# Kernel tuning notes

Hardware: AMD Instinct MI355X
Metric: run time of the kernel (lower is better)

## Reference

```python
import jax, jax.numpy as jnp
import numpy as np

B, M, N, P, H, W, D, DIMG, NH = 32, 2048, 512, 16, 640, 640, 256, 384, 8
PD = 3 * P * P  # 768 flattened patch dim


def layer_norm(x, g, b, eps=1e-5):
    mu = x.mean(-1, keepdims=True)
    var = ((x - mu) ** 2).mean(-1, keepdims=True)
    return (x - mu) * jax.lax.rsqrt(var + eps) * g + b


def get_patches(img, kpts, patch):
    # img [B,3,H,W], kpts [B,N,2] (x,y), NaN rows -> NaN patches
    Bb, C, Hh, Ww = img.shape
    half = patch // 2
    safe = jnp.nan_to_num(kpts, nan=0.0)
    ctr = jnp.round(safe).astype(jnp.int32)
    x0 = jnp.clip(ctr[..., 0] - half, 0, Ww - patch)
    y0 = jnp.clip(ctr[..., 1] - half, 0, Hh - patch)
    offs = jnp.arange(patch)
    ys = y0[..., None] + offs  # [B,N,P]
    xs = x0[..., None] + offs  # [B,N,P]

    def ext(im_b, ys_b, xs_b):
        p = im_b[:, ys_b[:, :, None], xs_b[:, None, :]]  # [C,N,P,P]
        return jnp.transpose(p, (1, 0, 2, 3))  # [N,C,P,P]

    patches = jax.vmap(ext)(img, ys, xs)  # [B,N,C,P,P]
    invalid = jnp.isnan(kpts).any(-1)
    return jnp.where(invalid[:, :, None, None, None], jnp.nan, patches)


def setup_inputs() -> dict:
    key = jax.random.key(0)
    ks = jax.random.split(key, 16)
    im0 = jax.random.uniform(ks[0], (B, 3, H, W), jnp.float32)
    im1 = jax.random.uniform(ks[1], (B, 3, H, W), jnp.float32)
    wh = jnp.array([W - 1.0, H - 1.0], jnp.float32)
    kpts0 = jax.random.uniform(ks[2], (B, M, 2), jnp.float32) * wh
    kpts1 = jax.random.uniform(ks[3], (B, M, 2), jnp.float32) * wh
    scores0 = jax.random.uniform(ks[4], (B, M), jnp.float32)
    scores1 = jax.random.uniform(ks[5], (B, M), jnp.float32)
    image_embs = jax.random.normal(ks[6], (B, DIMG), jnp.float32)
    m0 = jax.random.randint(ks[7], (B, N), 0, M)
    m1 = jax.random.randint(ks[8], (B, N), -300, M)
    m1 = jnp.where(m1 < 0, -1, m1)
    sorted_matches = jnp.stack([m0, m1], axis=-1).astype(jnp.int32)
    s = 0.02
    params = dict(
        ln1_g=jnp.ones((PD,), jnp.float32), ln1_b=jnp.zeros((PD,), jnp.float32),
        W_pe=jax.random.normal(ks[9], (D - 1, PD), jnp.float32) * s,
        b_pe=jnp.zeros((D - 1,), jnp.float32),
        ln2_g=jnp.ones((D - 1,), jnp.float32), ln2_b=jnp.zeros((D - 1,), jnp.float32),
        W_proj=jax.random.normal(ks[10], (D, DIMG), jnp.float32) * s,
        b_proj=jnp.zeros((D,), jnp.float32),
        in_w=jax.random.normal(ks[11], (3 * D, D), jnp.float32) * s,
        in_b=jnp.zeros((3 * D,), jnp.float32),
        out_w=jax.random.normal(ks[12], (D, D), jnp.float32) * s,
        out_b=jnp.zeros((D,), jnp.float32),
        W_fc=jax.random.normal(ks[13], (6, D), jnp.float32) * s,
        b_fc=jnp.zeros((6,), jnp.float32),
    )
    return dict(im0=im0, im1=im1, kpts0=kpts0, kpts1=kpts1, scores0=scores0,
                scores1=scores1, image_embs=image_embs,
                sorted_matches=sorted_matches, **params)


def reference(im0, im1, kpts0, kpts1, scores0, scores1, image_embs,
              sorted_matches, ln1_g, ln1_b, W_pe, b_pe, ln2_g, ln2_b,
              W_proj, b_proj, in_w, in_b, out_w, out_b, W_fc, b_fc):
    im0 = jnp.clip(im0, 0.0, 1.0)
    im1 = jnp.clip(im1, 0.0, 1.0)
    m0 = sorted_matches[..., 0]
    m1 = sorted_matches[..., 1]
    valid = m1 > -1  # [B,N]
    m0c = jnp.clip(m0, 0, M - 1)
    m1c = jnp.clip(m1, 0, M - 1)
    # vectorized masked gather with NaN padding (replaces the double python loop)
    g0 = jnp.take_along_axis(kpts0, m0c[..., None], axis=1)  # [B,N,2]
    g1 = jnp.take_along_axis(kpts1, m1c[..., None], axis=1)
    k0v = jnp.where(valid[..., None], g0, jnp.nan)
    k1v = jnp.where(valid[..., None], g1, jnp.nan)
    s0v = jnp.where(valid, jnp.take_along_axis(scores0, m0c, axis=1), 0.0)
    s1v = jnp.where(valid, jnp.take_along_axis(scores1, m1c, axis=1), 0.0)
    p0 = jnp.nan_to_num(get_patches(im0, k0v, P), nan=-1.0)  # [B,N,3,P,P]
    p1 = jnp.nan_to_num(get_patches(im1, k1v, P), nan=-1.0)
    patches = jnp.concatenate([p0, p1], axis=1)  # [B,2N,3,P,P]
    flat = patches.reshape(B, 2 * N, PD)
    e = layer_norm(flat, ln1_g, ln1_b)
    e = e @ W_pe.T + b_pe
    e = layer_norm(e, ln2_g, ln2_b)  # [B,2N,D-1]
    scores = jnp.concatenate([s0v, s1v], axis=1)  # [B,2N]
    pe = jnp.concatenate([e, scores[..., None]], axis=-1)  # [B,2N,D]
    # motion estimator: cross-attn, query = projected image embedding
    q = image_embs @ W_proj.T + b_proj  # [B,D]
    Wq, Wk, Wv = in_w[:D], in_w[D:2 * D], in_w[2 * D:]
    bq, bk, bv = in_b[:D], in_b[D:2 * D], in_b[2 * D:]
    dh = D // NH
    qh = (q @ Wq.T + bq).reshape(B, 1, NH, dh)
    kh = (pe @ Wk.T + bk).reshape(B, 2 * N, NH, dh)
    vh = (pe @ Wv.T + bv).reshape(B, 2 * N, NH, dh)
    scale = 1.0 / np.sqrt(dh).astype(np.float32)
    att = jnp.einsum('bqhd,bkhd->bhqk', qh, kh) * scale
    a = jax.nn.softmax(att, axis=-1)
    o = jnp.einsum('bhqk,bkhd->bqhd', a, vh).reshape(B, 1, D)
    o = o @ out_w.T + out_b
    out = (o @ W_fc.T + b_fc).reshape(B, 6)
    return out
```

## Files before the change

### kernel.cpp

```cpp
#include <hip/hip_runtime.h>
#include <math.h>

#define BB 32
#define MM 2048
#define NN 512
#define PSZ 16
#define HH 640
#define WW 640
#define DD 256
#define DIMG_ 384
#define NHEADS 8
#define PD_ 768
#define TWO_N 1024
#define ROWS_TOT (BB * TWO_N)
#define CHCT 32

typedef short bf16x8 __attribute__((ext_vector_type(8)));
typedef float f32x4  __attribute__((ext_vector_type(4)));

__device__ __forceinline__ unsigned short f2bf(float x) {
  unsigned int u = __float_as_uint(x);
  u = (u + 0x7FFF + ((u >> 16) & 1)) >> 16;
  return (unsigned short)u;
}
__device__ __forceinline__ float bf2f(unsigned short h) {
  return __uint_as_float(((unsigned int)h) << 16);
}

__device__ __forceinline__ void gload_lds16(const void* g, void* l) {
  __builtin_amdgcn_global_load_lds(
      (const __attribute__((address_space(1))) void*)g,
      (__attribute__((address_space(3))) void*)l, 16, 0, 0);
}

__global__ __launch_bounds__(256) void prep_extract_kernel(
    const float* __restrict__ W_pe,
    unsigned short* __restrict__ Whi, unsigned short* __restrict__ Wlo,
    const float* __restrict__ image_embs,
    const float* __restrict__ W_proj, const float* __restrict__ b_proj,
    const float* __restrict__ in_w,   const float* __restrict__ in_b,
    const float* __restrict__ b_pe,
    const float* __restrict__ ln2_g, const float* __restrict__ ln2_b,
    unsigned short* __restrict__ Vhi, unsigned short* __restrict__ Vlo,
    float* __restrict__ Pc,
    const float* __restrict__ im0, const float* __restrict__ im1,
    const float* __restrict__ kpts0, const float* __restrict__ kpts1,
    const float* __restrict__ scores0, const float* __restrict__ scores1,
    const int*   __restrict__ sorted_matches,
    const float* __restrict__ ln1_g, const float* __restrict__ ln1_b,
    unsigned short* __restrict__ Ahi, unsigned short* __restrict__ Alo,
    float* __restrict__ score_all)
{
  __shared__ float q1[DD];
  __shared__ float q2s[DD];
  __shared__ float u_sh[NHEADS][DD];
  __shared__ float gu_sh[DD][NHEADS];
  __shared__ float sred[NHEADS][3][4];
  const int t = threadIdx.x;

  if (blockIdx.x < 768) {
    const int idx = blockIdx.x * 256 + t;
    const int row = idx / PD_;
    float v = (row < 255) ? W_pe[idx] : 0.0f;
    const unsigned short h = f2bf(v);
    Whi[idx] = h;
    Wlo[idx] = f2bf(v - bf2f(h));
    return;
  }

  if (blockIdx.x < 800) {
    const int b = blockIdx.x - 768;
    {
      const float4* emb = (const float4*)(image_embs + (size_t)b * DIMG_);
      const float4* wr  = (const float4*)(W_proj + (size_t)t * DIMG_);
      float a = b_proj[t];
      #pragma unroll 4
      for (int i = 0; i < DIMG_ / 4; ++i) {
        const float4 e4 = emb[i], w4 = wr[i];
        a += e4.x * w4.x + e4.y * w4.y + e4.z * w4.z + e4.w * w4.w;
      }
      q1[t] = a;
    }
    __syncthreads();
    {
      const float4* wr = (const float4*)(in_w + (size_t)t * DD);
      const float4* qq = (const float4*)q1;
      float a = in_b[t];
      #pragma unroll 4
      for (int i = 0; i < DD / 4; ++i) {
        const float4 q4 = qq[i], w4 = wr[i];
        a += q4.x * w4.x + q4.y * w4.y + q4.z * w4.z + q4.w * w4.w;
      }
      q2s[t] = a;
    }
    __syncthreads();
    #pragma unroll
    for (int h = 0; h < NHEADS; ++h) {
      float s = 0.0f;
      #pragma unroll 8
      for (int i = 0; i < 32; ++i)
        s += q2s[h * 32 + i] * in_w[(size_t)(DD + h * 32 + i) * DD + t];
      u_sh[h][t] = s;
    }
    float ubv = 0.0f;
    if (t < NHEADS) {
      for (int i = 0; i < 32; ++i) ubv += q2s[t * 32 + i] * in_b[DD + t * 32 + i];
    }
    __syncthreads();

    const bool cvld = (t < 255);
    const float g_c = cvld ? ln2_g[t] : 0.0f;
    const float bb_c = cvld ? ln2_b[t] : 0.0f;
    const float pp_c = cvld ? b_pe[t]  : 0.0f;
    const int wv = t >> 6, ln = t & 63;
    #pragma unroll
    for (int h = 0; h < NHEADS; ++h) {
      const float u_c = u_sh[h][t];
      const float gu  = g_c * u_c;
      gu_sh[t][h] = gu;
      float x1 = gu, x2 = bb_c * u_c, x3 = pp_c * gu;
      #pragma unroll
      for (int m = 32; m; m >>= 1) {
        x1 += __shfl_xor(x1, m); x2 += __shfl_xor(x2, m); x3 += __shfl_xor(x3, m);
      }
      if (ln == 0) { sred[h][0][wv] = x1; sred[h][1][wv] = x2; sred[h][2][wv] = x3; }
    }
    __syncthreads();
    if (t < NHEADS) {
      const float S1 = sred[t][0][0] + sred[t][0][1] + sred[t][0][2] + sred[t][0][3];
      const float S2 = sred[t][1][0] + sred[t][1][1] + sred[t][1][2] + sred[t][1][3];
      const float S3 = sred[t][2][0] + sred[t][2][1] + sred[t][2][2] + sred[t][2][3];
      float* pc = Pc + b * 40;
      pc[t]      = S1;
      pc[8 + t]  = S2;
      pc[16 + t] = S3;
      pc[24 + t] = u_sh[t][255];
      pc[32 + t] = ubv;
    }

    #pragma unroll
    for (int kk = 0; kk < 3; ++kk) {
      const int k = t + 256 * kk;
      float vh[NHEADS] = {0, 0, 0, 0, 0, 0, 0, 0};
      for (int c = 0; c < 255; ++c) {
        const float wv_ = W_pe[(size_t)c * PD_ + k];
        const float4 g0 = *(const float4*)&gu_sh[c][0];
        const float4 g1 = *(const float4*)&gu_sh[c][4];
        vh[0] += wv_ * g0.x; vh[1] += wv_ * g0.y; vh[2] += wv_ * g0.z; vh[3] += wv_ * g0.w;
        vh[4] += wv_ * g1.x; vh[5] += wv_ * g1.y; vh[6] += wv_ * g1.z; vh[7] += wv_ * g1.w;
      }
      #pragma unroll
      for (int h = 0; h < NHEADS; ++h) {
        const unsigned short hi = f2bf(vh[h]);
        Vhi[((size_t)b * 16 + h) * PD_ + k] = hi;
        Vlo[((size_t)b * 16 + h) * PD_ + k] = f2bf(vh[h] - bf2f(hi));
      }
      #pragma unroll
      for (int h = NHEADS; h < 16; ++h) {
        Vhi[((size_t)b * 16 + h) * PD_ + k] = 0;
        Vlo[((size_t)b * 16 + h) * PD_ + k] = 0;
      }
    }
    return;
  }

  const int L  = t & 63;
  const long gp = (long)(blockIdx.x - 800) * 4 + (t >> 6);
  const int b   = (int)(gp >> 10);
  const int n2  = (int)(gp & 1023);
  const bool side1 = (n2 >= NN);
  const float* img  = side1 ? im1 : im0;
  const float* kpts = side1 ? kpts1 : kpts0;
  const float* scrs = side1 ? scores1 : scores0;

  const int n  = side1 ? (n2 - NN) : n2;
  const int m0 = sorted_matches[((size_t)b * NN + n) * 2 + 0];
  const int m1 = sorted_matches[((size_t)b * NN + n) * 2 + 1];
  const bool valid = (m1 > -1);
  int midx = side1 ? m1 : m0;
  midx = min(max(midx, 0), MM - 1);
  const float kx = kpts[((size_t)b * MM + midx) * 2 + 0];
  const float ky = kpts[((size_t)b * MM + midx) * 2 + 1];
  const int x0 = min(max((int)rintf(kx) - 8, 0), WW - PSZ);
  const int y0 = min(max((int)rintf(ky) - 8, 0), HH - PSZ);

  float v[12];
  if (valid) {
    const size_t imb = (size_t)b * 3 * HH * WW;
    const int px = (2 * L) & 15;
    #pragma unroll
    for (int j = 0; j < 6; ++j) {
      const int p0 = 2 * L + 128 * j;
      const int c  = p0 >> 8;
      const int py = (p0 >> 4) & 15;
      const float* rp = img + imb + ((size_t)c * HH + y0 + py) * WW + x0 + px;
      v[2 * j]     = fminf(fmaxf(rp[0], 0.0f), 1.0f);
      v[2 * j + 1] = fminf(fmaxf(rp[1], 0.0f), 1.0f);
    }
  } else {
    #pragma unroll
    for (int i = 0; i < 12; ++i) v[i] = -1.0f;
  }

  float s = 0.0f, ss = 0.0f;
  #pragma unroll
  for (int i = 0; i < 12; ++i) { s += v[i]; ss += v[i] * v[i]; }
  #pragma unroll
  for (int m = 32; m; m >>= 1) { s += __shfl_xor(s, m); ss += __shfl_xor(ss, m); }
  const float mu  = s * (1.0f / 768.0f);
  const float var = ss * (1.0f / 768.0f) - mu * mu;
  const float rs  = 1.0f / sqrtf(var + 1e-5f);

  unsigned int* AhiW = (unsigned int*)(Ahi + gp * PD_);
  unsigned int* AloW = (unsigned int*)(Alo + gp * PD_);
  #pragma unroll
  for (int j = 0; j < 6; ++j) {
    const int p0 = 2 * L + 128 * j;
    const float y0e = (v[2 * j]     - mu) * rs * ln1_g[p0]     + ln1_b[p0];
    const float y1e = (v[2 * j + 1] - mu) * rs * ln1_g[p0 + 1] + ln1_b[p0 + 1];
    const unsigned short h0 = f2bf(y0e), h1 = f2bf(y1e);
    AhiW[p0 >> 1] = (unsigned int)h0 | ((unsigned int)h1 << 16);
    const unsigned short l0 = f2bf(y0e - bf2f(h0));
    const unsigned short l1 = f2bf(y1e - bf2f(h1));
    AloW[p0 >> 1] = (unsigned int)l0 | ((unsigned int)l1 << 16);
  }
  if (L == 0) {
    score_all[gp] = valid ? scrs[(size_t)b * MM + midx] : 0.0f;
  }
}

__global__ __launch_bounds__(256, 2) void gemm_fused_kernel(
    const unsigned short* __restrict__ Ahi, const unsigned short* __restrict__ Alo,
    const unsigned short* __restrict__ Whi, const unsigned short* __restrict__ Wlo,
    const unsigned short* __restrict__ Vhi, const unsigned short* __restrict__ Vlo,
    const float* __restrict__ b_pe,
    const float* __restrict__ ln2_g, const float* __restrict__ ln2_b,
    const float* __restrict__ score_all,
    const float* __restrict__ Pc,
    float* __restrict__ pe, float* __restrict__ lt)
{
  __shared__ __align__(16) unsigned short sm[21504];
  const int t = threadIdx.x;
  const int w = t >> 6, L = t & 63;
  const int mt = blockIdx.x;
  const int bidx = mt >> 4;

  const int rr   = L >> 2;
  const int q_st = (L & 3) ^ ((L >> 4) & 3);
  const int lane_m = L & 15, quad = L >> 4;
  const int swz = quad ^ (lane_m >> 2);

  const unsigned short* gsrc[11];
  int ldst[11];
  #pragma unroll
  for (int c = 0; c < 11; ++c) {
    const int cc = w + 4 * c;
    const unsigned short* sp = Ahi; long rb = 0; int dst = 0;
    if (cc < 4)       { sp = Ahi; rb = (long)mt * 64 + cc * 16;       dst = cc * 512; }
    else if (cc < 8)  { sp = Alo; rb = (long)mt * 64 + (cc - 4) * 16; dst = 2048 + (cc - 4) * 512; }
    else if (cc < 25) { const int r0 = (cc - 8) * 16;
                        sp = (r0 < 256) ? (Whi + (long)r0 * PD_)
                                        : (Vhi + (long)bidx * 16 * PD_);
                        dst = 4096 + (cc - 8) * 512; }
    else if (cc < 42) { const int r0 = (cc - 25) * 16;
                        sp = (r0 < 256) ? (Wlo + (long)r0 * PD_)
                                        : (Vlo + (long)bidx * 16 * PD_);
                        dst = 12800 + (cc - 25) * 512; }
    gsrc[c] = sp + (rb + rr) * (long)PD_ + q_st * 8;
    ldst[c] = dst;
  }
  const int CNT = (w < 2) ? 11 : 10;
  const int JW  = (w == 3) ? 5 : 4;

  f32x4 acc[4][5];
  #pragma unroll
  for (int i = 0; i < 4; ++i)
    #pragma unroll
    for (int j = 0; j < 5; ++j) acc[i][j] = (f32x4){0.f, 0.f, 0.f, 0.f};

  for (int ks = 0; ks < PD_ / 32; ++ks) {
    const int k0 = ks * 32;
    __syncthreads();
    #pragma unroll
    for (int c = 0; c < 11; ++c)
      if (c < CNT) gload_lds16(gsrc[c] + k0, sm + ldst[c]);
    __syncthreads();

    bf16x8 ah[4], al[4];
    #pragma unroll
    for (int i = 0; i < 4; ++i) {
      const int offa = (i * 16 + lane_m) * 32 + swz * 8;
      ah[i] = *(const bf16x8*)(sm + offa);
      al[i] = *(const bf16x8*)(sm + 2048 + offa);
    }
    #pragma unroll
    for (int j = 0; j < 5; ++j) {
      if (j < JW) {
        const int offb = (w * 64 + j * 16 + lane_m) * 32 + swz * 8;
        const bf16x8 bh = *(const bf16x8*)(sm + 4096 + offb);
        const bf16x8 bl = *(const bf16x8*)(sm + 12800 + offb);
        #pragma unroll
        for (int i = 0; i < 4; ++i) {
          acc[i][j] = __builtin_amdgcn_mfma_f32_16x16x32_bf16(ah[i], bh, acc[i][j], 0, 0, 0);
          acc[i][j] = __builtin_amdgcn_mfma_f32_16x16x32_bf16(ah[i], bl, acc[i][j], 0, 0, 0);
          acc[i][j] = __builtin_amdgcn_mfma_f32_16x16x32_bf16(al[i], bh, acc[i][j], 0, 0, 0);
        }
      }
    }
  }

  __syncthreads();
  float* const fs = (float*)sm;
  float p4[4], g4[4], b4[4];
  #pragma unroll
  for (int j = 0; j < 4; ++j) {
    const int c = w * 64 + j * 16 + lane_m;
    const bool cv = (c < 255);
    p4[j] = cv ? b_pe[c]  : 0.0f;
    g4[j] = cv ? ln2_g[c] : 0.0f;
    b4[j] = cv ? ln2_b[c] : 0.0f;
  }
  float sv[16], qv[16];
  #pragma unroll
  for (int i = 0; i < 4; ++i)
    #pragma unroll
    for (int v = 0; v < 4; ++v) {
      float s = 0.0f, q = 0.0f;
      #pragma unroll
      for (int j = 0; j < 4; ++j) {
        const float x = acc[i][j][v] + p4[j];
        s += x; q += x * x;
      }
      sv[i * 4 + v] = s; qv[i * 4 + v] = q;
    }
  #pragma unroll
  for (int iv = 0; iv < 16; ++iv) {
    #pragma unroll
    for (int m = 1; m <= 8; m <<= 1) {
      sv[iv] += __shfl_xor(sv[iv], m);
      qv[iv] += __shfl_xor(qv[iv], m);
    }
  }
  if (lane_m == 0) {
    #pragma unroll
    for (int i = 0; i < 4; ++i)
      #pragma unroll
      for (int v = 0; v < 4; ++v) {
        const int row = i * 16 + quad * 4 + v;
        fs[w * 64 + row]       = sv[i * 4 + v];
        fs[256 + w * 64 + row] = qv[i * 4 + v];
      }
  }
  __syncthreads();
  if (t < 64) {
    const float S  = fs[t] + fs[64 + t] + fs[128 + t] + fs[192 + t];
    const float SS = fs[256 + t] + fs[320 + t] + fs[384 + t] + fs[448 + t];
    const float mu  = S * (1.0f / 255.0f);
    const float var = SS * (1.0f / 255.0f) - mu * mu;
    fs[512 + t] = mu;
    fs[576 + t] = 1.0f / sqrtf(var + 1e-5f);
  }
  __syncthreads();

  float S1 = 0, S2 = 0, S3 = 0, u255 = 0, ubias = 0;
  if (w == 3 && lane_m < NHEADS) {
    const float* pc = Pc + bidx * 40;
    S1 = pc[lane_m]; S2 = pc[8 + lane_m]; S3 = pc[16 + lane_m];
    u255 = pc[24 + lane_m]; ubias = pc[32 + lane_m];
  }

  #pragma unroll
  for (int i = 0; i < 4; ++i)
    #pragma unroll
    for (int v = 0; v < 4; ++v) {
      const int row = i * 16 + quad * 4 + v;
      const long grow = (long)mt * 64 + row;
      const float mu = fs[512 + row];
      const float rs = fs[576 + row];
      float sc = 0.0f;
      if (w == 3) sc = score_all[grow];
      float* rowp = pe + grow * DD + w * 64 + lane_m;
      #pragma unroll
      for (int j = 0; j < 4; ++j) {
        const int c = w * 64 + j * 16 + lane_m;
        const float y = (c < 255)
            ? (acc[i][j][v] + p4[j] - mu) * rs * g4[j] + b4[j]
            : sc;
        rowp[j * 16] = y;
      }
      if (w == 3 && lane_m < NHEADS) {
        const float T = acc[i][4][v];
        const float d = rs * (T + S3 - mu * S1) + S2 + sc * u255;
        lt[grow * NHEADS + lane_m] = (d + ubias) * 0.17677669529663687f;
      }
    }
}

__global__ __launch_bounds__(256) void softmax_kernel(
    const float* __restrict__ lt, float* __restrict__ prg)
{
  const int b = blockIdx.x, t = threadIdx.x;
  const int h = t >> 5, l = t & 31;
  const float* base = lt + (size_t)b * TWO_N * NHEADS + h;
  float v[32];
  float mx = -1e30f;
  #pragma unroll 8
  for (int i = 0; i < 32; ++i) { v[i] = base[(l + 32 * i) * NHEADS]; mx = fmaxf(mx, v[i]); }
  #pragma unroll
  for (int m = 16; m; m >>= 1) mx = fmaxf(mx, __shfl_xor(mx, m, 32));
  float sm = 0.0f;
  #pragma unroll 8
  for (int i = 0; i < 32; ++i) { v[i] = expf(v[i] - mx); sm += v[i]; }
  #pragma unroll
  for (int m = 16; m; m >>= 1) sm += __shfl_xor(sm, m, 32);
  const float inv = 1.0f / sm;
  float* out = prg + (size_t)b * TWO_N * NHEADS + h;
  #pragma unroll 8
  for (int i = 0; i < 32; ++i) out[(l + 32 * i) * NHEADS] = v[i] * inv;
}

__global__ __launch_bounds__(256) void ctx_kernel(
    const float* __restrict__ pe, const float* __restrict__ prg,
    float* __restrict__ ctxp)
{
  __shared__ __align__(16) float prc[32 * NHEADS];
  const int b = blockIdx.x, ch = blockIdx.y, t = threadIdx.x;
  prc[t] = prg[((size_t)b * TWO_N + ch * 32) * NHEADS + t];
  __syncthreads();

  const float* peb = pe + ((size_t)b * TWO_N + ch * 32) * DD;
  float acc[NHEADS] = {0, 0, 0, 0, 0, 0, 0, 0};
  #pragma unroll 4
  for (int k = 0; k < 32; ++k) {
    const float v = peb[(size_t)k * DD + t];
    const float4 a0 = *(const float4*)&prc[k * NHEADS];
    const float4 a1 = *(const float4*)&prc[k * NHEADS + 4];
    acc[0] += a0.x * v; acc[1] += a0.y * v; acc[2] += a0.z * v; acc[3] += a0.w * v;
    acc[4] += a1.x * v; acc[5] += a1.y * v; acc[6] += a1.z * v; acc[7] += a1.w * v;
  }
  #pragma unroll
  for (int h = 0; h < NHEADS; ++h)
    ctxp[(((size_t)b * CHCT + ch) * NHEADS + h) * DD + t] = acc[h];
}

__global__ __launch_bounds__(256) void final_kernel(
    const float* __restrict__ ctxp,
    const float* __restrict__ in_w,  const float* __restrict__ in_b,
    const float* __restrict__ out_w, const float* __restrict__ out_b,
    const float* __restrict__ W_fc,  const float* __restrict__ b_fc,
    float* __restrict__ outp)
{
  __shared__ __align__(16) float ctx_sh[NHEADS * DD];
  __shared__ __align__(16) float o_sh[DD], o2_sh[DD];
  const int t = threadIdx.x;
  const int b = blockIdx.x;

  #pragma unroll
  for (int h = 0; h < NHEADS; ++h) {
    float s = 0.0f;
    #pragma unroll
    for (int ch = 0; ch < CHCT; ++ch)
      s += ctxp[(((size_t)b * CHCT + ch) * NHEADS + h) * DD + t];
    ctx_sh[h * DD + t] = s;
  }
  __syncthreads();
  {
    const float4* wv = (const float4*)(in_w + (size_t)(2 * DD + t) * DD);
    const float4* cx = (const float4*)(ctx_sh + (t >> 5) * DD);
    float o1 = in_b[2 * DD + t];
    #pragma unroll 4
    for (int j = 0; j < DD / 4; ++j) {
      const float4 w4 = wv[j], c4 = cx[j];
      o1 += w4.x * c4.x + w4.y * c4.y + w4.z * c4.z + w4.w * c4.w;
    }
    o_sh[t] = o1;
  }
  __syncthreads();
  {
    const float4* wr = (const float4*)(out_w + (size_t)t * DD);
    const float4* oo = (const float4*)o_sh;
    float o2 = out_b[t];
    #pragma unroll 4
    for (int j = 0; j < DD / 4; ++j) {
      const float4 w4 = wr[j], c4 = oo[j];
      o2 += w4.x * c4.x + w4.y * c4.y + w4.z * c4.z + w4.w * c4.w;
    }
    o2_sh[t] = o2;
  }
  __syncthreads();
  if (t < 6) {
    const float4* wr = (const float4*)(W_fc + (size_t)t * DD);
    const float4* oo = (const float4*)o2_sh;
    float r = b_fc[t];
    for (int j = 0; j < DD / 4; ++j) {
      const float4 w4 = wr[j], c4 = oo[j];
      r += w4.x * c4.x + w4.y * c4.y + w4.z * c4.z + w4.w * c4.w;
    }
    outp[b * 6 + t] = r;
  }
}

extern "C" void kernel_launch(void* const* d_in, const int* in_sizes, int n_in,
                              void* d_out, int out_size, void* d_ws, size_t ws_size,
                              hipStream_t stream) {
  const float* im0       = (const float*)d_in[0];
  const float* im1       = (const float*)d_in[1];
  const float* kpts0     = (const float*)d_in[2];
  const float* kpts1     = (const float*)d_in[3];
  const float* scores0   = (const float*)d_in[4];
  const float* scores1   = (const float*)d_in[5];
  const float* image_embs= (const float*)d_in[6];
  const int*   smatch    = (const int*)d_in[7];
  const float* ln1_g     = (const float*)d_in[8];
  const float* ln1_b     = (const float*)d_in[9];
  const float* W_pe      = (const float*)d_in[10];
  const float* b_pe      = (const float*)d_in[11];
  const float* ln2_g     = (const float*)d_in[12];
  const float* ln2_b     = (const float*)d_in[13];
  const float* W_proj    = (const float*)d_in[14];
  const float* b_proj    = (const float*)d_in[15];
  const float* in_w      = (const float*)d_in[16];
  const float* in_b      = (const float*)d_in[17];
  const float* out_w     = (const float*)d_in[18];
  const float* out_b     = (const float*)d_in[19];
  const float* W_fc      = (const float*)d_in[20];
  const float* b_fc      = (const float*)d_in[21];

  char* ws = (char*)d_ws;
  size_t off = 0;
  float* epe   = (float*)(ws + off); off += (size_t)ROWS_TOT * DD * 4;
  float* score = (float*)(ws + off); off += (size_t)ROWS_TOT * 4;
  float* lt    = (float*)(ws + off); off += (size_t)BB * TWO_N * NHEADS * 4;
  float* prg   = (float*)(ws + off); off += (size_t)BB * TWO_N * NHEADS * 4;
  float* ctxp  = (float*)(ws + off); off += (size_t)BB * CHCT * NHEADS * DD * 4;
  float* Pc    = (float*)(ws + off); off += (size_t)BB * 40 * 4;
  off = (off + 1023) & ~(size_t)1023;
  unsigned short* Whi = (unsigned short*)(ws + off); off += (size_t)256 * PD_ * 2;
  unsigned short* Wlo = (unsigned short*)(ws + off); off += (size_t)256 * PD_ * 2;
  unsigned short* Vhi = (unsigned short*)(ws + off); off += (size_t)BB * 16 * PD_ * 2;
  unsigned short* Vlo = (unsigned short*)(ws + off); off += (size_t)BB * 16 * PD_ * 2;
  off = (off + 1023) & ~(size_t)1023;
  unsigned short* Ahi = (unsigned short*)(ws + off); off += (size_t)ROWS_TOT * PD_ * 2;
  unsigned short* Alo = (unsigned short*)(ws + off); off += (size_t)ROWS_TOT * PD_ * 2;

  prep_extract_kernel<<<800 + ROWS_TOT / 4, 256, 0, stream>>>(
      W_pe, Whi, Wlo, image_embs, W_proj, b_proj, in_w, in_b,
      b_pe, ln2_g, ln2_b, Vhi, Vlo, Pc,
      im0, im1, kpts0, kpts1, scores0, scores1, smatch,
      ln1_g, ln1_b, Ahi, Alo, score);
  gemm_fused_kernel<<<ROWS_TOT / 64, 256, 0, stream>>>(
      Ahi, Alo, Whi, Wlo, Vhi, Vlo, b_pe, ln2_g, ln2_b, score, Pc, epe, lt);
  softmax_kernel<<<BB, 256, 0, stream>>>(lt, prg);
  ctx_kernel<<<dim3(BB, CHCT), 256, 0, stream>>>(epe, prg, ctxp);
  final_kernel<<<BB, 256, 0, stream>>>(ctxp, in_w, in_b, out_w, out_b,
                                       W_fc, b_fc, (float*)d_out);
}
```

Baseline: 545.0 us.

## Compute attention logits in separate kernel instead of folding into GEMM

Removes the algebraic folding of the key projection into extra GEMM columns (Vhi/Vlo and the Pc constants) and the expensive per-batch V precompute in the prep kernel. Logits are instead computed by a new kernel that dots each stored pe row with per-head u vectors. This shrinks the GEMM's B tile from 272 to 256 columns and balances its warps. The cost is an extra launch plus a second full read of the pe buffer.

```diff
diff --git a/kernel.cpp b/kernel.cpp
--- a/kernel.cpp
+++ b/kernel.cpp
@@ -39,10 +39,7 @@
     const float* __restrict__ image_embs,
     const float* __restrict__ W_proj, const float* __restrict__ b_proj,
     const float* __restrict__ in_w,   const float* __restrict__ in_b,
-    const float* __restrict__ b_pe,
-    const float* __restrict__ ln2_g, const float* __restrict__ ln2_b,
-    unsigned short* __restrict__ Vhi, unsigned short* __restrict__ Vlo,
-    float* __restrict__ Pc,
+    float* __restrict__ u_out, float* __restrict__ bias_out,
     const float* __restrict__ im0, const float* __restrict__ im1,
     const float* __restrict__ kpts0, const float* __restrict__ kpts1,
     const float* __restrict__ scores0, const float* __restrict__ scores1,
@@ -52,10 +49,7 @@
     float* __restrict__ score_all)
 {
   __shared__ float q1[DD];
-  __shared__ float q2s[DD];
-  __shared__ float u_sh[NHEADS][DD];
-  __shared__ float gu_sh[DD][NHEADS];
-  __shared__ float sred[NHEADS][3][4];
+  __shared__ float q2[DD];
   const int t = threadIdx.x;
 
   if (blockIdx.x < 768) {
@@ -91,7 +85,7 @@
         const float4 q4 = qq[i], w4 = wr[i];
         a += q4.x * w4.x + q4.y * w4.y + q4.z * w4.z + q4.w * w4.w;
       }
-      q2s[t] = a;
+      q2[t] = a;
     }
     __syncthreads();
     #pragma unroll
@@ -99,67 +93,13 @@
       float s = 0.0f;
       #pragma unroll 8
       for (int i = 0; i < 32; ++i)
-        s += q2s[h * 32 + i] * in_w[(size_t)(DD + h * 32 + i) * DD + t];
-      u_sh[h][t] = s;
-    }
-    float ubv = 0.0f;
+        s += q2[h * 32 + i] * in_w[(size_t)(DD + h * 32 + i) * DD + t];
+      u_out[((size_t)b * NHEADS + h) * DD + t] = s;
+    }
     if (t < NHEADS) {
-      for (int i = 0; i < 32; ++i) ubv += q2s[t * 32 + i] * in_b[DD + t * 32 + i];
-    }
-    __syncthreads();
-
-    const bool cvld = (t < 255);
-    const float g_c = cvld ? ln2_g[t] : 0.0f;
-    const float bb_c = cvld ? ln2_b[t] : 0.0f;
-    const float pp_c = cvld ? b_pe[t]  : 0.0f;
-    const int wv = t >> 6, ln = t & 63;
-    #pragma unroll
-    for (int h = 0; h < NHEADS; ++h) {
-      const float u_c = u_sh[h][t];
-      const float gu  = g_c * u_c;
-      gu_sh[t][h] = gu;
-      float x1 = gu, x2 = bb_c * u_c, x3 = pp_c * gu;
-      #pragma unroll
-      for (int m = 32; m; m >>= 1) {
-        x1 += __shfl_xor(x1, m); x2 += __shfl_xor(x2, m); x3 += __shfl_xor(x3, m);
-      }
-      if (ln == 0) { sred[h][0][wv] = x1; sred[h][1][wv] = x2; sred[h][2][wv] = x3; }
-    }
-    __syncthreads();
-    if (t < NHEADS) {
-      const float S1 = sred[t][0][0] + sred[t][0][1] + sred[t][0][2] + sred[t][0][3];
-      const float S2 = sred[t][1][0] + sred[t][1][1] + sred[t][1][2] + sred[t][1][3];
-      const float S3 = sred[t][2][0] + sred[t][2][1] + sred[t][2][2] + sred[t][2][3];
-      float* pc = Pc + b * 40;
-      pc[t]      = S1;
-      pc[8 + t]  = S2;
-      pc[16 + t] = S3;
-      pc[24 + t] = u_sh[t][255];
-      pc[32 + t] = ubv;
-    }
-
-    #pragma unroll
-    for (int kk = 0; kk < 3; ++kk) {
-      const int k = t + 256 * kk;
-      float vh[NHEADS] = {0, 0, 0, 0, 0, 0, 0, 0};
-      for (int c = 0; c < 255; ++c) {
-        const float wv_ = W_pe[(size_t)c * PD_ + k];
-        const float4 g0 = *(const float4*)&gu_sh[c][0];
-        const float4 g1 = *(const float4*)&gu_sh[c][4];
-        vh[0] += wv_ * g0.x; vh[1] += wv_ * g0.y; vh[2] += wv_ * g0.z; vh[3] += wv_ * g0.w;
-        vh[4] += wv_ * g1.x; vh[5] += wv_ * g1.y; vh[6] += wv_ * g1.z; vh[7] += wv_ * g1.w;
-      }
-      #pragma unroll
-      for (int h = 0; h < NHEADS; ++h) {
-        const unsigned short hi = f2bf(vh[h]);
-        Vhi[((size_t)b * 16 + h) * PD_ + k] = hi;
-        Vlo[((size_t)b * 16 + h) * PD_ + k] = f2bf(vh[h] - bf2f(hi));
-      }
-      #pragma unroll
-      for (int h = NHEADS; h < 16; ++h) {
-        Vhi[((size_t)b * 16 + h) * PD_ + k] = 0;
-        Vlo[((size_t)b * 16 + h) * PD_ + k] = 0;
-      }
+      float s = 0.0f;
+      for (int i = 0; i < 32; ++i) s += q2[t * 32 + i] * in_b[DD + t * 32 + i];
+      bias_out[b * NHEADS + t] = s;
     }
     return;
   }
@@ -232,58 +172,47 @@
 __global__ __launch_bounds__(256, 2) void gemm_fused_kernel(
     const unsigned short* __restrict__ Ahi, const unsigned short* __restrict__ Alo,
     const unsigned short* __restrict__ Whi, const unsigned short* __restrict__ Wlo,
-    const unsigned short* __restrict__ Vhi, const unsigned short* __restrict__ Vlo,
     const float* __restrict__ b_pe,
     const float* __restrict__ ln2_g, const float* __restrict__ ln2_b,
     const float* __restrict__ score_all,
-    const float* __restrict__ Pc,
-    float* __restrict__ pe, float* __restrict__ lt)
+    float* __restrict__ pe)
 {
-  __shared__ __align__(16) unsigned short sm[21504];
+  __shared__ __align__(16) unsigned short sm[20480];
   const int t = threadIdx.x;
   const int w = t >> 6, L = t & 63;
   const int mt = blockIdx.x;
-  const int bidx = mt >> 4;
 
   const int rr   = L >> 2;
   const int q_st = (L & 3) ^ ((L >> 4) & 3);
   const int lane_m = L & 15, quad = L >> 4;
   const int swz = quad ^ (lane_m >> 2);
 
-  const unsigned short* gsrc[11];
-  int ldst[11];
-  #pragma unroll
-  for (int c = 0; c < 11; ++c) {
+  const unsigned short* gsrc[10];
+  int ldst[10];
+  #pragma unroll
+  for (int c = 0; c < 10; ++c) {
     const int cc = w + 4 * c;
-    const unsigned short* sp = Ahi; long rb = 0; int dst = 0;
+    const unsigned short* sp; long rb; int dst;
     if (cc < 4)       { sp = Ahi; rb = (long)mt * 64 + cc * 16;       dst = cc * 512; }
     else if (cc < 8)  { sp = Alo; rb = (long)mt * 64 + (cc - 4) * 16; dst = 2048 + (cc - 4) * 512; }
-    else if (cc < 25) { const int r0 = (cc - 8) * 16;
-                        sp = (r0 < 256) ? (Whi + (long)r0 * PD_)
-                                        : (Vhi + (long)bidx * 16 * PD_);
-                        dst = 4096 + (cc - 8) * 512; }
-    else if (cc < 42) { const int r0 = (cc - 25) * 16;
-                        sp = (r0 < 256) ? (Wlo + (long)r0 * PD_)
-                                        : (Vlo + (long)bidx * 16 * PD_);
-                        dst = 12800 + (cc - 25) * 512; }
+    else if (cc < 24) { sp = Whi; rb = (long)(cc - 8) * 16;           dst = 4096 + (cc - 8) * 512; }
+    else              { sp = Wlo; rb = (long)(cc - 24) * 16;          dst = 12288 + (cc - 24) * 512; }
     gsrc[c] = sp + (rb + rr) * (long)PD_ + q_st * 8;
     ldst[c] = dst;
   }
-  const int CNT = (w < 2) ? 11 : 10;
-  const int JW  = (w == 3) ? 5 : 4;
-
-  f32x4 acc[4][5];
+
+  f32x4 acc[4][4];
   #pragma unroll
   for (int i = 0; i < 4; ++i)
     #pragma unroll
-    for (int j = 0; j < 5; ++j) acc[i][j] = (f32x4){0.f, 0.f, 0.f, 0.f};
+    for (int j = 0; j < 4; ++j) acc[i][j] = (f32x4){0.f, 0.f, 0.f, 0.f};
 
   for (int ks = 0; ks < PD_ / 32; ++ks) {
     const int k0 = ks * 32;
     __syncthreads();
     #pragma unroll
-    for (int c = 0; c < 11; ++c)
-      if (c < CNT) gload_lds16(gsrc[c] + k0, sm + ldst[c]);
+    for (int c = 0; c < 10; ++c)
+      gload_lds16(gsrc[c] + k0, sm + ldst[c]);
     __syncthreads();
 
     bf16x8 ah[4], al[4];
@@ -294,17 +223,15 @@
       al[i] = *(const bf16x8*)(sm + 2048 + offa);
     }
     #pragma unroll
-    for (int j = 0; j < 5; ++j) {
-      if (j < JW) {
-        const int offb = (w * 64 + j * 16 + lane_m) * 32 + swz * 8;
-        const bf16x8 bh = *(const bf16x8*)(sm + 4096 + offb);
-        const bf16x8 bl = *(const bf16x8*)(sm + 12800 + offb);
-        #pragma unroll
-        for (int i = 0; i < 4; ++i) {
-          acc[i][j] = __builtin_amdgcn_mfma_f32_16x16x32_bf16(ah[i], bh, acc[i][j], 0, 0, 0);
-          acc[i][j] = __builtin_amdgcn_mfma_f32_16x16x32_bf16(ah[i], bl, acc[i][j], 0, 0, 0);
-          acc[i][j] = __builtin_amdgcn_mfma_f32_16x16x32_bf16(al[i], bh, acc[i][j], 0, 0, 0);
-        }
+    for (int j = 0; j < 4; ++j) {
+      const int offb = (w * 64 + j * 16 + lane_m) * 32 + swz * 8;
+      const bf16x8 bh = *(const bf16x8*)(sm + 4096 + offb);
+      const bf16x8 bl = *(const bf16x8*)(sm + 12288 + offb);
+      #pragma unroll
+      for (int i = 0; i < 4; ++i) {
+        acc[i][j] = __builtin_amdgcn_mfma_f32_16x16x32_bf16(ah[i], bh, acc[i][j], 0, 0, 0);
+        acc[i][j] = __builtin_amdgcn_mfma_f32_16x16x32_bf16(ah[i], bl, acc[i][j], 0, 0, 0);
+        acc[i][j] = __builtin_amdgcn_mfma_f32_16x16x32_bf16(al[i], bh, acc[i][j], 0, 0, 0);
       }
     }
   }
@@ -361,13 +288,6 @@
     fs[576 + t] = 1.0f / sqrtf(var + 1e-5f);
   }
   __syncthreads();
-
-  float S1 = 0, S2 = 0, S3 = 0, u255 = 0, ubias = 0;
-  if (w == 3 && lane_m < NHEADS) {
-    const float* pc = Pc + bidx * 40;
-    S1 = pc[lane_m]; S2 = pc[8 + lane_m]; S3 = pc[16 + lane_m];
-    u255 = pc[24 + lane_m]; ubias = pc[32 + lane_m];
-  }
 
   #pragma unroll
   for (int i = 0; i < 4; ++i)
@@ -388,12 +308,49 @@
             : sc;
         rowp[j * 16] = y;
       }
-      if (w == 3 && lane_m < NHEADS) {
-        const float T = acc[i][4][v];
-        const float d = rs * (T + S3 - mu * S1) + S2 + sc * u255;
-        lt[grow * NHEADS + lane_m] = (d + ubias) * 0.17677669529663687f;
-      }
-    }
+    }
+}
+
+__global__ __launch_bounds__(256) void logits_kernel(
+    const float* __restrict__ pe,
+    const float* __restrict__ u, const float* __restrict__ ubias,
+    float* __restrict__ lt)
+{
+  __shared__ __align__(16) float u_sh[NHEADS * DD];
+  __shared__ float ub_sh[NHEADS];
+  const int t = threadIdx.x;
+  const long row0 = (long)blockIdx.x * 8;
+  const int b = (int)(row0 >> 10);
+
+  const float* ub = u + (size_t)b * NHEADS * DD;
+  #pragma unroll
+  for (int i = 0; i < 8; ++i) u_sh[t + 256 * i] = ub[t + 256 * i];
+  if (t < NHEADS) ub_sh[t] = ubias[b * NHEADS + t];
+  __syncthreads();
+
+  const int r = t >> 5, l = t & 31;
+  const long row = row0 + r;
+  const float4* pr4 = (const float4*)(pe + row * DD);
+  float d[NHEADS] = {0, 0, 0, 0, 0, 0, 0, 0};
+  #pragma unroll
+  for (int half = 0; half < 2; ++half) {
+    const float4 x = pr4[l + 32 * half];
+    #pragma unroll
+    for (int h = 0; h < NHEADS; ++h) {
+      const float4 uu = *(const float4*)&u_sh[h * DD + 4 * (l + 32 * half)];
+      d[h] += x.x * uu.x + x.y * uu.y + x.z * uu.z + x.w * uu.w;
+    }
+  }
+  #pragma unroll
+  for (int h = 0; h < NHEADS; ++h) {
+    #pragma unroll
+    for (int m = 16; m; m >>= 1) d[h] += __shfl_xor(d[h], m, 32);
+  }
+  if (l == 0) {
+    #pragma unroll
+    for (int h = 0; h < NHEADS; ++h)
+      lt[row * NHEADS + h] = (d[h] + ub_sh[h]) * 0.17677669529663687f;
+  }
 }
 
 __global__ __launch_bounds__(256) void softmax_kernel(
@@ -529,27 +486,27 @@
   char* ws = (char*)d_ws;
   size_t off = 0;
   float* epe   = (float*)(ws + off); off += (size_t)ROWS_TOT * DD * 4;
+  float* u     = (float*)(ws + off); off += (size_t)BB * NHEADS * DD * 4;
+  float* ubias = (float*)(ws + off); off += (size_t)BB * NHEADS * 4;
+  off = (off + 1023) & ~(size_t)1023;
   float* score = (float*)(ws + off); off += (size_t)ROWS_TOT * 4;
   float* lt    = (float*)(ws + off); off += (size_t)BB * TWO_N * NHEADS * 4;
   float* prg   = (float*)(ws + off); off += (size_t)BB * TWO_N * NHEADS * 4;
   float* ctxp  = (float*)(ws + off); off += (size_t)BB * CHCT * NHEADS * DD * 4;
-  float* Pc    = (float*)(ws + off); off += (size_t)BB * 40 * 4;
   off = (off + 1023) & ~(size_t)1023;
   unsigned short* Whi = (unsigned short*)(ws + off); off += (size_t)256 * PD_ * 2;
   unsigned short* Wlo = (unsigned short*)(ws + off); off += (size_t)256 * PD_ * 2;
-  unsigned short* Vhi = (unsigned short*)(ws + off); off += (size_t)BB * 16 * PD_ * 2;
-  unsigned short* Vlo = (unsigned short*)(ws + off); off += (size_t)BB * 16 * PD_ * 2;
   off = (off + 1023) & ~(size_t)1023;
   unsigned short* Ahi = (unsigned short*)(ws + off); off += (size_t)ROWS_TOT * PD_ * 2;
   unsigned short* Alo = (unsigned short*)(ws + off); off += (size_t)ROWS_TOT * PD_ * 2;
 
   prep_extract_kernel<<<800 + ROWS_TOT / 4, 256, 0, stream>>>(
-      W_pe, Whi, Wlo, image_embs, W_proj, b_proj, in_w, in_b,
-      b_pe, ln2_g, ln2_b, Vhi, Vlo, Pc,
+      W_pe, Whi, Wlo, image_embs, W_proj, b_proj, in_w, in_b, u, ubias,
       im0, im1, kpts0, kpts1, scores0, scores1, smatch,
       ln1_g, ln1_b, Ahi, Alo, score);
   gemm_fused_kernel<<<ROWS_TOT / 64, 256, 0, stream>>>(
-      Ahi, Alo, Whi, Wlo, Vhi, Vlo, b_pe, ln2_g, ln2_b, score, Pc, epe, lt);
+      Ahi, Alo, Whi, Wlo, b_pe, ln2_g, ln2_b, score, epe);
+  logits_kernel<<<ROWS_TOT / 8, 256, 0, stream>>>(epe, u, ubias, lt);
   softmax_kernel<<<BB, 256, 0, stream>>>(lt, prg);
   ctx_kernel<<<dim3(BB, CHCT), 256, 0, stream>>>(epe, prg, ctxp);
   final_kernel<<<BB, 256, 0, stream>>>(ctxp, in_w, in_b, out_w, out_b,
```

Result: faster. 473.1 us (-13.2%).
